# Kernel tuning notes

Hardware: AMD Instinct MI355X
Metric: run time of the kernel (lower is better)

Reference implementation:

```python
import jax, jax.numpy as jnp
import numpy as np

NUM_HEADS = 16
HEAD_DIM = 80
HIDDEN = 1280
SEQ = 3072
NUM_SEGS = 6  # 6 packed images of 512 patches each


def rotate_half(x):
    x1, x2 = jnp.split(x, 2, axis=-1)
    return jnp.concatenate([-x2, x1], axis=-1)


def setup_inputs() -> dict:
    key = jax.random.key(0)
    ks = jax.random.split(key, 6)
    hidden_states = jax.random.normal(ks[0], (SEQ, HIDDEN), dtype=jnp.float32)
    # RoPE tables as in Qwen-VL vision: freqs over half the head_dim, duplicated
    half = HEAD_DIM // 2
    inv_freq = 1.0 / (10000.0 ** (jnp.arange(half, dtype=jnp.float32) / half))
    pos = jnp.arange(SEQ, dtype=jnp.float32)[:, None]
    freqs = pos * inv_freq[None, :]                      # (SEQ, half)
    emb = jnp.concatenate([freqs, freqs], axis=-1)       # (SEQ, HEAD_DIM)
    cos = jnp.cos(emb)
    sin = jnp.sin(emb)
    # Packed segment boundaries: [0, 512, 1024, ..., 3072]
    cu_seqlens = jnp.arange(0, SEQ + 1, SEQ // NUM_SEGS, dtype=jnp.int32)
    scale = 0.02
    w_qkv = jax.random.normal(ks[1], (3 * HIDDEN, HIDDEN), dtype=jnp.float32) * scale
    b_qkv = jax.random.normal(ks[2], (3 * HIDDEN,), dtype=jnp.float32) * scale
    w_proj = jax.random.normal(ks[3], (HIDDEN, HIDDEN), dtype=jnp.float32) * scale
    b_proj = jax.random.normal(ks[4], (HIDDEN,), dtype=jnp.float32) * scale
    return {
        "hidden_states": hidden_states, "cos": cos, "sin": sin,
        "w_qkv": w_qkv, "b_qkv": b_qkv, "w_proj": w_proj, "b_proj": b_proj,
        "cu_seqlens": cu_seqlens,
    }


def reference(hidden_states, cos, sin, w_qkv, b_qkv, w_proj, b_proj, cu_seqlens):
    S, H = hidden_states.shape
    nh, hd = NUM_HEADS, H // NUM_HEADS

    # Fused QKV projection: (S, 3H) -> q, k, v each (S, nh, hd)
    qkv = hidden_states @ w_qkv.T + b_qkv
    qkv = qkv.reshape(S, 3, nh, hd)
    q, k, v = qkv[:, 0], qkv[:, 1], qkv[:, 2]

    # Inline RoPE on q/k (cos/sin broadcast over heads)
    c = cos[:, None, :]
    s = sin[:, None, :]
    q = q * c + rotate_half(q) * s
    k = k * c + rotate_half(k) * s

    # Original casts fp32 -> fp16 for the flash attention kernel
    q16 = q.astype(jnp.float16)
    k16 = k.astype(jnp.float16)
    v16 = v.astype(jnp.float16)

    # Varlen masking: tokens attend only within their own packed segment
    tok = jnp.arange(S)
    seg = jnp.searchsorted(cu_seqlens, tok, side="right")  # (S,)
    same_seg = seg[:, None] == seg[None, :]                 # (S, S)

    scale = hd ** (-0.5)
    # Scores accumulated in fp32 (as flash attention does internally)
    scores = jnp.einsum("qhd,khd->hqk", q16, k16,
                        preferred_element_type=jnp.float32) * scale
    scores = jnp.where(same_seg[None], scores, jnp.finfo(jnp.float32).min)
    weights = jax.nn.softmax(scores, axis=-1).astype(jnp.float16)  # (nh, S, S)

    attn = jnp.einsum("hqk,khd->qhd", weights, v16)  # (S, nh, hd) fp16
    attn = attn.astype(jnp.float32).reshape(S, H)
    return attn @ w_proj.T + b_proj
```

## Files before the change

### kernel.cpp

```cpp
#include <hip/hip_runtime.h>

typedef _Float16 f16;
typedef _Float16 half8 __attribute__((ext_vector_type(8)));
typedef _Float16 half4 __attribute__((ext_vector_type(4)));
typedef float f32x4 __attribute__((ext_vector_type(4)));

__device__ __forceinline__ void gld_lds16(const void* g, void* l) {
  __builtin_amdgcn_global_load_lds((const __attribute__((address_space(1))) void*)g,
                                   (__attribute__((address_space(3))) void*)l, 16, 0, 0);
}

template <int CTRL>
__device__ __forceinline__ float dppf(float x) {
  return __builtin_bit_cast(float,
      __builtin_amdgcn_mov_dpp(__builtin_bit_cast(int, x), CTRL, 0xf, 0xf, true));
}
__device__ __forceinline__ float dpp_max16(float v) {
  v = fmaxf(v, dppf<0xB1>(v));
  v = fmaxf(v, dppf<0x4E>(v));
  v = fmaxf(v, dppf<0x128>(v));
  v = fmaxf(v, dppf<0x140>(v));
  return v;
}
__device__ __forceinline__ float dpp_sum16(float v) {
  v += dppf<0xB1>(v);
  v += dppf<0x4E>(v);
  v += dppf<0x128>(v);
  v += dppf<0x140>(v);
  return v;
}

__global__ void cvt_all(const float* __restrict__ hid, const float* __restrict__ wq,
                        const float* __restrict__ wp, f16* __restrict__ hid16,
                        f16* __restrict__ wq16, f16* __restrict__ wp16) {
  int b = blockIdx.x;
  const float* in;
  f16* out;
  int i;
  if (b < 3840) { in = hid; out = hid16; i = b * 256 + threadIdx.x; }
  else if (b < 8640) { in = wq; out = wq16; i = (b - 3840) * 256 + threadIdx.x; }
  else { in = wp; out = wp16; i = (b - 8640) * 256 + threadIdx.x; }
  float4 v = ((const float4*)in)[i];
  half4 o;
  o.x = (f16)v.x; o.y = (f16)v.y; o.z = (f16)v.z; o.w = (f16)v.w;
  ((half4*)out)[i] = o;
}

__global__ __launch_bounds__(512, 2) void gemm240(const f16* __restrict__ A,
                                                  const f16* __restrict__ B,
                                                  const float* __restrict__ bias,
                                                  f16* __restrict__ C) {
  __shared__ f16 S[57344];
  char* Sb = (char*)S;
  const int tid = threadIdx.x, lane = tid & 63, wid = tid >> 6;
  const int lm = lane & 15, q4 = lane >> 4;
  const int wm = wid >> 2, wn = wid & 3;
  const int swz = ((int)blockIdx.x & 7) * 30 + ((int)blockIdx.x >> 3);
  const int bm = (swz % 12) * 256, bn = (swz / 12) * 192;

  const int ch = ((lane & 7) ^ (lane >> 3)) << 3;
  uint32_t aoff[4], boff[3];
#pragma unroll
  for (int q = 0; q < 4; q++)
    aoff[q] = (uint32_t)((bm + q * 64 + wid * 8 + (lane >> 3)) * 1280 + ch);
#pragma unroll
  for (int i = 0; i < 3; i++)
    boff[i] = (uint32_t)((bn + wid * 24 + i * 8 + (lane >> 3)) * 1280 + ch);

  const int xr = (lm & 7) << 4;
  int aro[2][2], bro[3][2];
#pragma unroll
  for (int f = 0; f < 2; f++)
#pragma unroll
    for (int ks = 0; ks < 2; ks++)
      aro[f][ks] = (wm * 32 + f * 16 + lm) * 128 + ((ks * 64 + q4 * 16) ^ xr);
#pragma unroll
  for (int nh = 0; nh < 3; nh++)
#pragma unroll
    for (int ks = 0; ks < 2; ks++)
      bro[nh][ks] = (nh * 64 + wn * 16 + lm) * 128 + ((ks * 64 + q4 * 16) ^ xr);

  f32x4 acc[8][3] = {};

  {
#pragma unroll
    for (int q = 0; q < 4; q++)
      gld_lds16(A + aoff[q], Sb + q * 8192 + wid * 1024);
#pragma unroll
    for (int i = 0; i < 3; i++)
      gld_lds16(B + boff[i], Sb + 65536 + (3 * wid + i) * 1024);
    gld_lds16(A + aoff[0] + 64, Sb + 32768 + wid * 1024);
    gld_lds16(A + aoff[1] + 64, Sb + 32768 + 8192 + wid * 1024);
#pragma unroll
    for (int i = 0; i < 3; i++)
      gld_lds16(B + boff[i] + 64, Sb + 65536 + 24576 + (3 * wid + i) * 1024);
    asm volatile("s_waitcnt vmcnt(5)" ::: "memory");
    __builtin_amdgcn_s_barrier();
  }

  constexpr int NT = 20;
  for (int t = 0; t < NT; ++t) {
    const int p = t & 1;
    char* Ab = Sb + p * 32768;
    char* Bb = Sb + 65536 + p * 24576;
    char* An = Sb + (p ^ 1) * 32768;
    const int k1 = (t + 1 < NT ? t + 1 : NT - 1) * 64;
    const int k2 = (t + 2 < NT ? t + 2 : NT - 1) * 64;

    half8 a0[2][2], a1[2][2], bf[3][2];
#pragma unroll
    for (int f = 0; f < 2; f++)
#pragma unroll
      for (int ks = 0; ks < 2; ks++) {
        a0[f][ks] = *(const half8*)(Ab + aro[f][ks]);
        a1[f][ks] = *(const half8*)(Ab + 8192 + aro[f][ks]);
      }
#pragma unroll
    for (int nh = 0; nh < 3; nh++)
#pragma unroll
      for (int ks = 0; ks < 2; ks++)
        bf[nh][ks] = *(const half8*)(Bb + bro[nh][ks]);
    gld_lds16(A + aoff[2] + k1, An + 2 * 8192 + wid * 1024);
    gld_lds16(A + aoff[3] + k1, An + 3 * 8192 + wid * 1024);
    __builtin_amdgcn_s_setprio(1);
#pragma unroll
    for (int ks = 0; ks < 2; ks++)
#pragma unroll
      for (int f = 0; f < 2; f++)
#pragma unroll
        for (int nh = 0; nh < 3; nh++) {
          acc[f][nh] =
              __builtin_amdgcn_mfma_f32_16x16x32_f16(a0[f][ks], bf[nh][ks], acc[f][nh], 0, 0, 0);
          acc[2 + f][nh] = __builtin_amdgcn_mfma_f32_16x16x32_f16(a1[f][ks], bf[nh][ks],
                                                                  acc[2 + f][nh], 0, 0, 0);
        }
    __builtin_amdgcn_s_setprio(0);
    __builtin_amdgcn_sched_barrier(0);
    asm volatile("s_waitcnt lgkmcnt(0)" ::: "memory");
    __builtin_amdgcn_s_barrier();

#pragma unroll
    for (int f = 0; f < 2; f++)
#pragma unroll
      for (int ks = 0; ks < 2; ks++) {
        a0[f][ks] = *(const half8*)(Ab + 16384 + aro[f][ks]);
        a1[f][ks] = *(const half8*)(Ab + 24576 + aro[f][ks]);
      }
    gld_lds16(A + aoff[0] + k2, Ab + wid * 1024);
    gld_lds16(A + aoff[1] + k2, Ab + 8192 + wid * 1024);
#pragma unroll
    for (int i = 0; i < 3; i++)
      gld_lds16(B + boff[i] + k2, Bb + (3 * wid + i) * 1024);
    __builtin_amdgcn_s_setprio(1);
#pragma unroll
    for (int ks = 0; ks < 2; ks++)
#pragma unroll
      for (int f = 0; f < 2; f++)
#pragma unroll
        for (int nh = 0; nh < 3; nh++) {
          acc[4 + f][nh] = __builtin_amdgcn_mfma_f32_16x16x32_f16(a0[f][ks], bf[nh][ks],
                                                                  acc[4 + f][nh], 0, 0, 0);
          acc[6 + f][nh] = __builtin_amdgcn_mfma_f32_16x16x32_f16(a1[f][ks], bf[nh][ks],
                                                                  acc[6 + f][nh], 0, 0, 0);
        }
    __builtin_amdgcn_s_setprio(0);
    __builtin_amdgcn_sched_barrier(0);
    asm volatile("s_waitcnt vmcnt(5)" ::: "memory");
    asm volatile("s_waitcnt lgkmcnt(0)" ::: "memory");
    __builtin_amdgcn_s_barrier();
  }

#pragma unroll
  for (int mf = 0; mf < 8; mf++)
#pragma unroll
    for (int nf = 0; nf < 3; nf++) {
      const int gc = bn + nf * 64 + wn * 16 + lm;
      const float bb = bias[gc];
      const int gr0 = bm + (mf >> 1) * 64 + wm * 32 + (mf & 1) * 16 + q4 * 4;
#pragma unroll
      for (int r = 0; r < 4; r++)
        C[(size_t)(gr0 + r) * 3840 + gc] = (f16)(acc[mf][nf][r] + bb);
    }
}

template <bool OUT_F16>
__global__ __launch_bounds__(256, 2) void gemm_bt64(const f16* __restrict__ A,
                                                    const f16* __restrict__ B,
                                                    const float* __restrict__ bias,
                                                    void* __restrict__ Cout,
                                                    int K, int lda, int ldb, int ldc) {
  __shared__ f16 As[64 * 32];
  __shared__ f16 Bs[128 * 32];
  const int tid = threadIdx.x, lane = tid & 63, wave = tid >> 6;
  const int bm = blockIdx.x * 64, bn = blockIdx.y * 128;
  const int wm = (wave & 1) * 32, wn = (wave >> 1) * 64;
  const int lm = lane & 15, kq = (lane >> 4) * 8;
  const int arow = tid >> 2, acol = (tid & 3) * 8;

  const f16* Ab = A + (size_t)(bm + arow) * lda + acol;
  const f16* Bb = B + (size_t)(bn + arow) * ldb + acol;
  f16* AsW = As + wave * 512;
  f16* BsW = Bs + wave * 512;

  f32x4 acc[2][4] = {};
  for (int k0 = 0; k0 < K; k0 += 32) {
    gld_lds16(Ab + k0, AsW);
    gld_lds16(Bb + k0, BsW);
    gld_lds16(Bb + (size_t)64 * ldb + k0, BsW + 2048);
    __syncthreads();
    half8 af[2], bf[4];
#pragma unroll
    for (int mt = 0; mt < 2; mt++) af[mt] = *(const half8*)&As[(wm + 16 * mt + lm) * 32 + kq];
#pragma unroll
    for (int nt = 0; nt < 4; nt++) bf[nt] = *(const half8*)&Bs[(wn + 16 * nt + lm) * 32 + kq];
#pragma unroll
    for (int mt = 0; mt < 2; mt++)
#pragma unroll
      for (int nt = 0; nt < 4; nt++)
        acc[mt][nt] = __builtin_amdgcn_mfma_f32_16x16x32_f16(af[mt], bf[nt], acc[mt][nt], 0, 0, 0);
    __syncthreads();
  }
  const int q4 = lane >> 4;
#pragma unroll
  for (int mt = 0; mt < 2; mt++)
#pragma unroll
    for (int nt = 0; nt < 4; nt++)
#pragma unroll
      for (int r = 0; r < 4; r++) {
        int gr = bm + wm + 16 * mt + 4 * q4 + r;
        int gc = bn + wn + 16 * nt + lm;
        float v = acc[mt][nt][r] + bias[gc];
        if (OUT_F16)
          ((f16*)Cout)[(size_t)gr * ldc + gc] = (f16)v;
        else
          ((float*)Cout)[(size_t)gr * ldc + gc] = v;
      }
}

__global__ void rope_transpose(f16* __restrict__ qkv, const float* __restrict__ cosb,
                               const float* __restrict__ sinb, f16* __restrict__ vt) {
  __shared__ f16 tile[64][72];
  const int b = blockIdx.x;
  if (b < 1920) {
    int idx = b * 256 + threadIdx.x;
    int c = idx % 5;
    int t = idx / 5;
    int h = t % 16; t /= 16;
    int qk = t & 1;
    int s = t >> 1;
    size_t base = (size_t)s * 3840 + qk * 1280 + h * 80 + c * 8;
    half8 x = *(half8*)&qkv[base];
    half8 y = *(half8*)&qkv[base + 40];
    const float* cp = cosb + s * 80 + c * 8;
    const float* sp = sinb + s * 80 + c * 8;
    half8 ox, oy;
#pragma unroll
    for (int i = 0; i < 8; i++) {
      float cs = cp[i], sn = sp[i];
      float xf = (float)x[i], yf = (float)y[i];
      ox[i] = (f16)(xf * cs - yf * sn);
      oy[i] = (f16)(yf * cs + xf * sn);
    }
    *(half8*)&qkv[base] = ox;
    *(half8*)&qkv[base + 40] = oy;
  } else {
    const int bb = b - 1920;
    const int bs = (bb % 48) * 64;
    const int bd = (bb / 48) * 64;
    const int r = threadIdx.x >> 2, c = (threadIdx.x & 3) * 16;
    *(uint4*)&tile[r][c] = *(const uint4*)&qkv[(size_t)(bs + r) * 3840 + 2560 + bd + c];
    *(uint4*)&tile[r][c + 8] = *(const uint4*)&qkv[(size_t)(bs + r) * 3840 + 2560 + bd + c + 8];
    __syncthreads();
    f16 tmp[16];
#pragma unroll
    for (int i = 0; i < 16; i++) tmp[i] = tile[c + i][r];
    *(uint4*)&vt[(size_t)(bd + r) * 3072 + bs + c] = *(uint4*)&tmp[0];
    *(uint4*)&vt[(size_t)(bd + r) * 3072 + bs + c + 8] = *(uint4*)&tmp[8];
  }
}

__global__ __launch_bounds__(256, 3) void flash_attn6(const f16* __restrict__ qkv,
                                                      const f16* __restrict__ vt,
                                                      f16* __restrict__ attn) {
  __shared__ f16 S[25088];
  const int tid = threadIdx.x, lane = tid & 63, wave = tid >> 6;
  const int lm = lane & 15, q4 = lane >> 4;
  const int h = blockIdx.x, g = blockIdx.z;
  const int qbase = g * 512 + blockIdx.y * 64 + wave * 16;
  f16* P = S + 20480 + wave * 1152;
  const half8 hz = {};

  const f16* qrow = qkv + (size_t)(qbase + lm) * 3840 + h * 80;
  half8 qf[3];
  qf[0] = *(const half8*)(qrow + q4 * 8);
  qf[1] = *(const half8*)(qrow + 32 + q4 * 8);
  qf[2] = (q4 < 2) ? *(const half8*)(qrow + 64 + q4 * 8) : hz;

  const bool isK = wave < 2;
  const f16* gsrc = isK ? qkv : vt;
  const uint32_t gstep = isK ? (uint32_t)(64 * 3840) : 64u;
  const int cbase = (wave & 1) * 5;
  const uint32_t ldsoff = (isK ? 0u : 5120u) + (uint32_t)cbase * 512u;
  uint32_t goff[5];
#pragma unroll
  for (int i = 0; i < 5; i++) {
    int t = (cbase + i) * 1024 + lane * 16;
    if (isK) {
      int row = t / 160, colb = t % 160;
      goff[i] = (uint32_t)((g * 512 + row) * 3840 + 1280 + h * 80 + (colb >> 1));
    } else {
      int vd = t >> 7, vsb = t & 127;
      int vsrc = vsb ^ ((vd & 7) << 4);
      goff[i] = (uint32_t)((h * 80 + vd) * 3072 + g * 512 + (vsrc >> 1));
    }
  }

  f32x4 oacc[5] = {};
  float mprev[4] = {-1e30f, -1e30f, -1e30f, -1e30f};
  float lsum[4] = {0.f, 0.f, 0.f, 0.f};
  const float sc = 0.11180339887498949f * 1.4426950408889634f;

#pragma unroll
  for (int i = 0; i < 5; i++) gld_lds16(gsrc + goff[i], S + ldsoff + i * 512);
  __syncthreads();

  for (int jj = 0; jj < 8; jj++) {
    const int p = jj & 1;
    f16* Kb = S + p * 10240;
    f16* Vb = Kb + 5120;
    if (jj < 7) {
#pragma unroll
      for (int i = 0; i < 5; i++)
        gld_lds16(gsrc + goff[i] + (uint32_t)(jj + 1) * gstep,
                  S + (p ^ 1) * 10240 + ldsoff + i * 512);
    }

    f32x4 sacc[4] = {};
#pragma unroll
    for (int ks = 0; ks < 3; ks++) {
      half8 bk[4];
#pragma unroll
      for (int nt = 0; nt < 4; nt++)
        bk[nt] = (ks < 2 || q4 < 2)
                     ? *(const half8*)&Kb[(16 * nt + lm) * 80 + 32 * ks + q4 * 8]
                     : hz;
#pragma unroll
      for (int nt = 0; nt < 4; nt++)
        sacc[nt] = __builtin_amdgcn_mfma_f32_16x16x32_f16(qf[ks], bk[nt], sacc[nt], 0, 0, 0);
    }

    float mnew[4], alpha[4], rs[4];
#pragma unroll
    for (int r = 0; r < 4; r++) {
      float v = fmaxf(fmaxf(sacc[0][r], sacc[1][r]), fmaxf(sacc[2][r], sacc[3][r]));
      v = dpp_max16(v);
      mnew[r] = fmaxf(mprev[r], v * sc);
      alpha[r] = __builtin_exp2f(mprev[r] - mnew[r]);
      mprev[r] = mnew[r];
      rs[r] = 0.f;
    }
#pragma unroll
    for (int nt = 0; nt < 4; nt++)
#pragma unroll
      for (int r = 0; r < 4; r++) {
        float pp = __builtin_exp2f(sacc[nt][r] * sc - mnew[r]);
        sacc[nt][r] = pp;
        rs[r] += pp;
      }
#pragma unroll
    for (int r = 0; r < 4; r++) {
      float v = dpp_sum16(rs[r]);
      lsum[r] = alpha[r] * lsum[r] + v;
#pragma unroll
      for (int nt2 = 0; nt2 < 5; nt2++) oacc[nt2][r] *= alpha[r];
    }

#pragma unroll
    for (int nt = 0; nt < 4; nt++)
#pragma unroll
      for (int r = 0; r < 4; r++)
        P[(4 * q4 + r) * 72 + 16 * nt + lm] = (f16)sacc[nt][r];

#pragma unroll
    for (int ks = 0; ks < 2; ks++) {
      half8 ap = *(const half8*)&P[lm * 72 + ks * 32 + q4 * 8];
      half8 bv[5];
#pragma unroll
      for (int nt2 = 0; nt2 < 5; nt2++) {
        int row = 16 * nt2 + lm;
        bv[nt2] = *(const half8*)&Vb[row * 64 + ((ks * 32 + q4 * 8) ^ ((row & 7) << 3))];
      }
#pragma unroll
      for (int nt2 = 0; nt2 < 5; nt2++)
        oacc[nt2] = __builtin_amdgcn_mfma_f32_16x16x32_f16(ap, bv[nt2], oacc[nt2], 0, 0, 0);
    }

    __syncthreads();
  }

#pragma unroll
  for (int r = 0; r < 4; r++) {
    float inv = 1.0f / lsum[r];
    int s = qbase + 4 * q4 + r;
#pragma unroll
    for (int nt2 = 0; nt2 < 5; nt2++)
      attn[(size_t)s * 1280 + h * 80 + 16 * nt2 + lm] = (f16)(oacc[nt2][r] * inv);
  }
}

extern "C" void kernel_launch(void* const* d_in, const int* in_sizes, int n_in,
                              void* d_out, int out_size, void* d_ws, size_t ws_size,
                              hipStream_t stream) {
  const float* hidden = (const float*)d_in[0];
  const float* cosb   = (const float*)d_in[1];
  const float* sinb   = (const float*)d_in[2];
  const float* w_qkv  = (const float*)d_in[3];
  const float* b_qkv  = (const float*)d_in[4];
  const float* w_proj = (const float*)d_in[5];
  const float* b_proj = (const float*)d_in[6];

  char* ws = (char*)d_ws;
  f16* hidden16 = (f16*)(ws + 0);
  f16* wqkv16   = (f16*)(ws + 7864320);
  f16* wproj16  = (f16*)(ws + 17694720);
  f16* qkv16    = (f16*)(ws + 20971520);
  f16* attn16   = (f16*)(ws + 44564480);
  f16* vt16     = hidden16;

  cvt_all<<<10240, 256, 0, stream>>>(hidden, w_qkv, w_proj, hidden16, wqkv16, wproj16);

  gemm240<<<240, 512, 0, stream>>>(hidden16, wqkv16, b_qkv, qkv16);

  rope_transpose<<<2880, 256, 0, stream>>>(qkv16, cosb, sinb, vt16);

  flash_attn6<<<dim3(16, 8, 6), 256, 0, stream>>>(qkv16, vt16, attn16);

  gemm_bt64<false><<<dim3(48, 10), 256, 0, stream>>>(attn16, wproj16, b_proj, d_out,
                                                     1280, 1280, 1280, 1280);
}
```

Before: 189.0 us.

## Retile QKV GEMM to 128x192 blocks with 4 waves and 480 workgroups

The QKV projection GEMM now uses 128x192 output tiles per block with 256 threads (4 waves, each computing 64x96), instead of 256x192 tiles with 512 threads. The grid doubles from 240 to 480 workgroups, which fills the 256 CUs more evenly than 240 blocks did. Each wave now holds more B fragments per A fragment, and the tail prefetches are made conditional instead of clamping to the last tile, with a full vmcnt(0) drain at the end. Per-block LDS shrinks, but more blocks re-load the B tiles, which raises global and L2 traffic.

```diff
diff --git a/kernel.cpp b/kernel.cpp
--- a/kernel.cpp
+++ b/kernel.cpp
@@ -46,94 +46,90 @@
   ((half4*)out)[i] = o;
 }
 
-__global__ __launch_bounds__(512, 2) void gemm240(const f16* __restrict__ A,
+__global__ __launch_bounds__(256, 2) void gemm240(const f16* __restrict__ A,
                                                   const f16* __restrict__ B,
                                                   const float* __restrict__ bias,
                                                   f16* __restrict__ C) {
-  __shared__ f16 S[57344];
+  __shared__ f16 S[40960];
   char* Sb = (char*)S;
   const int tid = threadIdx.x, lane = tid & 63, wid = tid >> 6;
   const int lm = lane & 15, q4 = lane >> 4;
-  const int wm = wid >> 2, wn = wid & 3;
-  const int swz = ((int)blockIdx.x & 7) * 30 + ((int)blockIdx.x >> 3);
-  const int bm = (swz % 12) * 256, bn = (swz / 12) * 192;
+  const int wm = wid >> 1, wn = wid & 1;
+  const int swz = ((int)blockIdx.x & 7) * 60 + ((int)blockIdx.x >> 3);
+  const int bm = (swz % 24) * 128, bn = (swz / 24) * 192;
 
   const int ch = ((lane & 7) ^ (lane >> 3)) << 3;
-  uint32_t aoff[4], boff[3];
-#pragma unroll
-  for (int q = 0; q < 4; q++)
-    aoff[q] = (uint32_t)((bm + q * 64 + wid * 8 + (lane >> 3)) * 1280 + ch);
-#pragma unroll
-  for (int i = 0; i < 3; i++)
-    boff[i] = (uint32_t)((bn + wid * 24 + i * 8 + (lane >> 3)) * 1280 + ch);
+  uint32_t aoff[4], boff[6];
+#pragma unroll
+  for (int j = 0; j < 4; j++)
+    aoff[j] = (uint32_t)((bm + (j * 4 + wid) * 8 + (lane >> 3)) * 1280 + ch);
+#pragma unroll
+  for (int i = 0; i < 6; i++)
+    boff[i] = (uint32_t)((bn + wid * 48 + i * 8 + (lane >> 3)) * 1280 + ch);
 
   const int xr = (lm & 7) << 4;
-  int aro[2][2], bro[3][2];
-#pragma unroll
-  for (int f = 0; f < 2; f++)
+  int aro[4][2], bro[6][2];
+#pragma unroll
+  for (int f = 0; f < 4; f++)
 #pragma unroll
     for (int ks = 0; ks < 2; ks++)
-      aro[f][ks] = (wm * 32 + f * 16 + lm) * 128 + ((ks * 64 + q4 * 16) ^ xr);
-#pragma unroll
-  for (int nh = 0; nh < 3; nh++)
+      aro[f][ks] = (wm * 64 + f * 16 + lm) * 128 + ((ks * 64 + q4 * 16) ^ xr);
+#pragma unroll
+  for (int n = 0; n < 6; n++)
 #pragma unroll
     for (int ks = 0; ks < 2; ks++)
-      bro[nh][ks] = (nh * 64 + wn * 16 + lm) * 128 + ((ks * 64 + q4 * 16) ^ xr);
-
-  f32x4 acc[8][3] = {};
+      bro[n][ks] = (wn * 96 + n * 16 + lm) * 128 + ((ks * 64 + q4 * 16) ^ xr);
+
+  f32x4 acc[4][6] = {};
 
   {
 #pragma unroll
-    for (int q = 0; q < 4; q++)
-      gld_lds16(A + aoff[q], Sb + q * 8192 + wid * 1024);
-#pragma unroll
-    for (int i = 0; i < 3; i++)
-      gld_lds16(B + boff[i], Sb + 65536 + (3 * wid + i) * 1024);
-    gld_lds16(A + aoff[0] + 64, Sb + 32768 + wid * 1024);
-    gld_lds16(A + aoff[1] + 64, Sb + 32768 + 8192 + wid * 1024);
-#pragma unroll
-    for (int i = 0; i < 3; i++)
-      gld_lds16(B + boff[i] + 64, Sb + 65536 + 24576 + (3 * wid + i) * 1024);
-    asm volatile("s_waitcnt vmcnt(5)" ::: "memory");
+    for (int j = 0; j < 4; j++)
+      gld_lds16(A + aoff[j], Sb + (j * 4 + wid) * 1024);
+#pragma unroll
+    for (int i = 0; i < 6; i++)
+      gld_lds16(B + boff[i], Sb + 32768 + (wid * 6 + i) * 1024);
+    gld_lds16(A + aoff[0] + 64, Sb + 16384 + wid * 1024);
+    gld_lds16(A + aoff[2] + 64, Sb + 16384 + (8 + wid) * 1024);
+#pragma unroll
+    for (int i = 0; i < 6; i++)
+      gld_lds16(B + boff[i] + 64, Sb + 32768 + 24576 + (wid * 6 + i) * 1024);
+    asm volatile("s_waitcnt vmcnt(8)" ::: "memory");
     __builtin_amdgcn_s_barrier();
   }
 
   constexpr int NT = 20;
   for (int t = 0; t < NT; ++t) {
     const int p = t & 1;
-    char* Ab = Sb + p * 32768;
-    char* Bb = Sb + 65536 + p * 24576;
-    char* An = Sb + (p ^ 1) * 32768;
-    const int k1 = (t + 1 < NT ? t + 1 : NT - 1) * 64;
-    const int k2 = (t + 2 < NT ? t + 2 : NT - 1) * 64;
-
-    half8 a0[2][2], a1[2][2], bf[3][2];
+    char* Ab = Sb + p * 16384;
+    char* Bb = Sb + 32768 + p * 24576;
+    char* An = Sb + (p ^ 1) * 16384;
+    const int k1 = (t + 1) * 64, k2 = (t + 2) * 64;
+
+    half8 a0[2][2], bf[6][2];
 #pragma unroll
     for (int f = 0; f < 2; f++)
 #pragma unroll
-      for (int ks = 0; ks < 2; ks++) {
+      for (int ks = 0; ks < 2; ks++)
         a0[f][ks] = *(const half8*)(Ab + aro[f][ks]);
-        a1[f][ks] = *(const half8*)(Ab + 8192 + aro[f][ks]);
-      }
-#pragma unroll
-    for (int nh = 0; nh < 3; nh++)
+#pragma unroll
+    for (int n = 0; n < 6; n++)
 #pragma unroll
       for (int ks = 0; ks < 2; ks++)
-        bf[nh][ks] = *(const half8*)(Bb + bro[nh][ks]);
-    gld_lds16(A + aoff[2] + k1, An + 2 * 8192 + wid * 1024);
-    gld_lds16(A + aoff[3] + k1, An + 3 * 8192 + wid * 1024);
+        bf[n][ks] = *(const half8*)(Bb + bro[n][ks]);
+    if (t + 1 < NT) {
+      gld_lds16(A + aoff[1] + k1, An + (4 + wid) * 1024);
+      gld_lds16(A + aoff[3] + k1, An + (12 + wid) * 1024);
+    }
     __builtin_amdgcn_s_setprio(1);
 #pragma unroll
     for (int ks = 0; ks < 2; ks++)
 #pragma unroll
       for (int f = 0; f < 2; f++)
 #pragma unroll
-        for (int nh = 0; nh < 3; nh++) {
-          acc[f][nh] =
-              __builtin_amdgcn_mfma_f32_16x16x32_f16(a0[f][ks], bf[nh][ks], acc[f][nh], 0, 0, 0);
-          acc[2 + f][nh] = __builtin_amdgcn_mfma_f32_16x16x32_f16(a1[f][ks], bf[nh][ks],
-                                                                  acc[2 + f][nh], 0, 0, 0);
-        }
+        for (int n = 0; n < 6; n++)
+          acc[f][n] =
+              __builtin_amdgcn_mfma_f32_16x16x32_f16(a0[f][ks], bf[n][ks], acc[f][n], 0, 0, 0);
     __builtin_amdgcn_s_setprio(0);
     __builtin_amdgcn_sched_barrier(0);
     asm volatile("s_waitcnt lgkmcnt(0)" ::: "memory");
@@ -142,44 +138,45 @@
 #pragma unroll
     for (int f = 0; f < 2; f++)
 #pragma unroll
-      for (int ks = 0; ks < 2; ks++) {
-        a0[f][ks] = *(const half8*)(Ab + 16384 + aro[f][ks]);
-        a1[f][ks] = *(const half8*)(Ab + 24576 + aro[f][ks]);
-      }
-    gld_lds16(A + aoff[0] + k2, Ab + wid * 1024);
-    gld_lds16(A + aoff[1] + k2, Ab + 8192 + wid * 1024);
-#pragma unroll
-    for (int i = 0; i < 3; i++)
-      gld_lds16(B + boff[i] + k2, Bb + (3 * wid + i) * 1024);
+      for (int ks = 0; ks < 2; ks++)
+        a0[f][ks] = *(const half8*)(Ab + aro[2 + f][ks]);
+    if (t + 2 < NT) {
+      gld_lds16(A + aoff[0] + k2, Ab + wid * 1024);
+      gld_lds16(A + aoff[2] + k2, Ab + (8 + wid) * 1024);
+#pragma unroll
+      for (int i = 0; i < 6; i++)
+        gld_lds16(B + boff[i] + k2, Bb + (wid * 6 + i) * 1024);
+    }
     __builtin_amdgcn_s_setprio(1);
 #pragma unroll
     for (int ks = 0; ks < 2; ks++)
 #pragma unroll
       for (int f = 0; f < 2; f++)
 #pragma unroll
-        for (int nh = 0; nh < 3; nh++) {
-          acc[4 + f][nh] = __builtin_amdgcn_mfma_f32_16x16x32_f16(a0[f][ks], bf[nh][ks],
-                                                                  acc[4 + f][nh], 0, 0, 0);
-          acc[6 + f][nh] = __builtin_amdgcn_mfma_f32_16x16x32_f16(a1[f][ks], bf[nh][ks],
-                                                                  acc[6 + f][nh], 0, 0, 0);
-        }
+        for (int n = 0; n < 6; n++)
+          acc[2 + f][n] = __builtin_amdgcn_mfma_f32_16x16x32_f16(a0[f][ks], bf[n][ks],
+                                                                 acc[2 + f][n], 0, 0, 0);
     __builtin_amdgcn_s_setprio(0);
     __builtin_amdgcn_sched_barrier(0);
-    asm volatile("s_waitcnt vmcnt(5)" ::: "memory");
+    if (t + 2 < NT) {
+      asm volatile("s_waitcnt vmcnt(8)" ::: "memory");
+    } else {
+      asm volatile("s_waitcnt vmcnt(0)" ::: "memory");
+    }
     asm volatile("s_waitcnt lgkmcnt(0)" ::: "memory");
     __builtin_amdgcn_s_barrier();
   }
 
 #pragma unroll
-  for (int mf = 0; mf < 8; mf++)
-#pragma unroll
-    for (int nf = 0; nf < 3; nf++) {
-      const int gc = bn + nf * 64 + wn * 16 + lm;
+  for (int f = 0; f < 4; f++)
+#pragma unroll
+    for (int n = 0; n < 6; n++) {
+      const int gc = bn + wn * 96 + n * 16 + lm;
       const float bb = bias[gc];
-      const int gr0 = bm + (mf >> 1) * 64 + wm * 32 + (mf & 1) * 16 + q4 * 4;
+      const int gr0 = bm + wm * 64 + f * 16 + q4 * 4;
 #pragma unroll
       for (int r = 0; r < 4; r++)
-        C[(size_t)(gr0 + r) * 3840 + gc] = (f16)(acc[mf][nf][r] + bb);
+        C[(size_t)(gr0 + r) * 3840 + gc] = (f16)(acc[f][n][r] + bb);
     }
 }
 
@@ -429,7 +426,7 @@
 
   cvt_all<<<10240, 256, 0, stream>>>(hidden, w_qkv, w_proj, hidden16, wqkv16, wproj16);
 
-  gemm240<<<240, 512, 0, stream>>>(hidden16, wqkv16, b_qkv, qkv16);
+  gemm240<<<480, 256, 0, stream>>>(hidden16, wqkv16, b_qkv, qkv16);
 
   rope_transpose<<<2880, 256, 0, stream>>>(qkv16, cosb, sinb, vt16);
 
```

Measured after the change: 186.0 us. About the same (-1.6%).
